# Kernel optimization log

Measured on AMD Instinct MI355X. Metric: run time of the kernel, lower is better.

The kernel has to match this reference:

```python
import jax, jax.numpy as jnp
import numpy as np
import math

B, T, Dm, H = 512, 64, 1024, 16
dh = Dm // H
CD, SD = 32, 256  # smolgen compress_dim, shared_dim
SCALE = 1.0 / math.sqrt(dh)
RES_SCALE = 1.0 / math.sqrt(2.0)  # n_layers=1
EPS = 1e-5


def _ln(v, g, b):
    m = jnp.mean(v, axis=-1, keepdims=True)
    var = jnp.mean(jnp.square(v - m), axis=-1, keepdims=True)
    return (v - m) * jax.lax.rsqrt(var + EPS) * g + b


def setup_inputs() -> dict:
    key = jax.random.key(0)
    ks = jax.random.split(key, 16)
    s = 0.02
    return {
        "x": jax.random.normal(ks[0], (B, T, Dm), jnp.float32),
        # weights stored (in, out); y = x @ W + b
        "Wq": jax.random.normal(ks[1], (Dm, Dm), jnp.float32) * s,
        "Wk": jax.random.normal(ks[2], (Dm, Dm), jnp.float32) * s,
        "Wv": jax.random.normal(ks[3], (Dm, Dm), jnp.float32) * s,
        "Wo_w": jax.random.normal(ks[4], (Dm, Dm), jnp.float32) * s,
        "Wo_b": jnp.zeros((Dm,), jnp.float32),
        "static_bias": jax.random.normal(ks[5], (H, T, T), jnp.float32) * s,
        "aQ": jax.random.normal(ks[6], (H, T, T, dh), jnp.float32) * s,
        "aK": jax.random.normal(ks[7], (H, T, T, dh), jnp.float32) * s,
        "aV": jax.random.normal(ks[8], (H, T, T, dh), jnp.float32) * s,
        # Smolgen params
        "pt_w": jax.random.normal(ks[9], (Dm, CD), jnp.float32) * s,
        "pt_b": jnp.zeros((CD,), jnp.float32),
        "pg_w": jax.random.normal(ks[10], (T * CD, SD), jnp.float32) * s,
        "pg_b": jnp.zeros((SD,), jnp.float32),
        "ph_w": jax.random.normal(ks[11], (SD, H * SD), jnp.float32) * s,
        "ph_b": jnp.zeros((H * SD,), jnp.float32),
        "ln1_g": jnp.ones((SD,), jnp.float32),
        "ln1_b": jnp.zeros((SD,), jnp.float32),
        "ln2_g": jnp.ones((SD,), jnp.float32),
        "ln2_b": jnp.zeros((SD,), jnp.float32),
        "shared_w": jax.random.normal(ks[12], (SD, T * T), jnp.float32) * s,
    }


def _smolgen(x, pt_w, pt_b, pg_w, pg_b, ph_w, ph_b, ln1_g, ln1_b, ln2_g, ln2_b, shared_w):
    z = x @ pt_w + pt_b                      # (B,T,CD)
    g = z.reshape(x.shape[0], T * CD) @ pg_w + pg_b  # (B,SD)
    g = _ln(jax.nn.silu(g), ln1_g, ln1_b)
    u = g @ ph_w + ph_b                      # (B,H*SD)
    u = jax.nn.silu(u).reshape(-1, H, SD)
    u = _ln(u, ln2_g, ln2_b)
    return (u @ shared_w).reshape(-1, H, T, T)


def reference(x, Wq, Wk, Wv, Wo_w, Wo_b, static_bias, aQ, aK, aV,
              pt_w, pt_b, pg_w, pg_b, ph_w, ph_b,
              ln1_g, ln1_b, ln2_g, ln2_b, shared_w):
    Bx = x.shape[0]
    Q = (x @ Wq).reshape(Bx, T, H, dh).transpose(0, 2, 1, 3)  # (B,H,T,dh)
    K = (x @ Wk).reshape(Bx, T, H, dh).transpose(0, 2, 1, 3)
    V = (x @ Wv).reshape(Bx, T, H, dh).transpose(0, 2, 1, 3)
    logits = jnp.einsum('bhtd,bhsd->bhts', Q, K) * SCALE
    logits = logits + static_bias[None]
    logits = logits + jnp.einsum('bhtd,htsd->bhts', Q, aK) * SCALE
    logits = logits + jnp.einsum('htsd,bhsd->bhts', aQ, K) * SCALE
    logits = logits + (jnp.einsum('htsd,htsd->hts', aQ, aK) * SCALE)[None]
    logits = logits + _smolgen(x, pt_w, pt_b, pg_w, pg_b, ph_w, ph_b,
                               ln1_g, ln1_b, ln2_g, ln2_b, shared_w)
    attn = jax.nn.softmax(logits, axis=-1)  # dropout = identity (eval mode)
    out = jnp.einsum('bhts,bhsd->bhtd', attn, V)
    out = out + jnp.einsum('bhts,htsd->bhtd', attn, aV)
    out = out.transpose(0, 2, 1, 3).reshape(Bx, T, Dm)
    return (out @ Wo_w + Wo_b) * RES_SCALE
```

## Files before the change

### kernel.cpp

```cpp
#include <hip/hip_runtime.h>
#include <cstdint>
#include <cstdio>

typedef unsigned short u16;
typedef __attribute__((ext_vector_type(8))) short s8v;
typedef __attribute__((ext_vector_type(4))) float f4v;
typedef __attribute__((ext_vector_type(4))) unsigned short u16x4;
typedef const __attribute__((address_space(1))) void* gas_p;
typedef __attribute__((address_space(3))) void* las_p;

#define DEV __device__ __forceinline__

static constexpr float SCALE_ = 0.125f;
static constexpr float RES_SCALE_ = 0.7071067811865475f;
static constexpr float EPS_ = 1e-5f;

DEV u16 f2bf(float f) {
  uint32_t u = __float_as_uint(f);
  u += 0x7fffu + ((u >> 16) & 1u);
  return (u16)(u >> 16);
}
DEV float bf2f(u16 h) { return __uint_as_float(((uint32_t)h) << 16); }

DEV f4v mfma16(s8v a, s8v b, f4v c) {
  return __builtin_amdgcn_mfma_f32_16x16x32_bf16(a, b, c, 0, 0, 0);
}

#define WAITVM4 asm volatile("s_waitcnt vmcnt(4)" ::: "memory")
#define WAITVM0 asm volatile("s_waitcnt vmcnt(0)" ::: "memory")
#define WAITLG0 asm volatile("s_waitcnt lgkmcnt(0)" ::: "memory")
#define SCHEDB  __builtin_amdgcn_sched_barrier(0)
#define BAR     __builtin_amdgcn_s_barrier()


__global__ void k_zero(float* __restrict__ p, long n) {
  long i = (long)blockIdx.x * blockDim.x + threadIdx.x;
  long stride = (long)gridDim.x * blockDim.x;
  for (; i < n; i += stride) p[i] = 0.f;
}

__global__ void k_cvt(const float* __restrict__ in, u16* __restrict__ out, long n4) {
  long i = (long)blockIdx.x * blockDim.x + threadIdx.x;
  long stride = (long)gridDim.x * blockDim.x;
  for (; i < n4; i += stride) {
    f4v v = *(const f4v*)&in[i * 4];
    u16x4 o;
    o.x = f2bf(v.x); o.y = f2bf(v.y); o.z = f2bf(v.z); o.w = f2bf(v.w);
    *(u16x4*)&out[i * 4] = o;
  }
}

__global__ void k_transpose(const float* __restrict__ in, u16* __restrict__ out, int K, int N) {
  __shared__ float tile[64][65];
  int kb = blockIdx.x * 64, nb = blockIdx.y * 64;
  for (int i = threadIdx.x; i < 4096; i += 256) {
    int r = i >> 6, c = i & 63;
    tile[r][c] = in[(long)(kb + r) * N + nb + c];
  }
  __syncthreads();
  for (int i = threadIdx.x; i < 4096; i += 256) {
    int c = i >> 6, r = i & 63;
    out[(long)(nb + c) * K + kb + r] = f2bf(tile[r][c]);
  }
}

__global__ void k_ptwt(const float* __restrict__ in, u16* __restrict__ out) {
  int idx = blockIdx.x * 256 + threadIdx.x;
  int n = idx >> 10, k = idx & 1023;
  out[idx] = f2bf(in[k * 32 + n]);
}

__global__ void k_avt(const float* __restrict__ aV, u16* __restrict__ aVt) {
  __shared__ float tile[64][65];
  int ht = blockIdx.x;
  const float* src = aV + (long)ht * 4096;
  for (int i = threadIdx.x; i < 4096; i += 256) {
    int s = i >> 6, d = i & 63;
    tile[s][d] = src[i];
  }
  __syncthreads();
  u16* dst = aVt + (long)ht * 4096;
  for (int i = threadIdx.x; i < 4096; i += 256) {
    int d = i >> 6, s = i & 63;
    dst[i] = f2bf(tile[s][d]);
  }
}

__global__ void k_extra(const float* __restrict__ sb, const float* __restrict__ aQ,
                        const float* __restrict__ aK, float* __restrict__ extra) {
  int idx = blockIdx.x * 256 + threadIdx.x;
  const float* q = aQ + (long)idx * 64;
  const float* k = aK + (long)idx * 64;
  float acc = 0.f;
#pragma unroll 8
  for (int d = 0; d < 64; d++) acc += q[d] * k[d];
  extra[idx] = sb[idx] + acc * SCALE_;
}

template <int EPI>
__launch_bounds__(512)
__global__ void k_gemm256(const u16* __restrict__ A, const u16* __restrict__ Bt,
                          void* __restrict__ Cv, const float* __restrict__ aux,
                          int M, int N, int K) {
  __shared__ u16 lds[65536];

  const int nwg = gridDim.x;
  int wg = blockIdx.x;
  if ((nwg & 7) == 0) wg = (wg & 7) * (nwg >> 3) + (wg >> 3);
  const int ntiles = N >> 8;
  const int mt = wg / ntiles, ntb = wg % ntiles;

  const int tid = threadIdx.x;
  const int lane = tid & 63, w = tid >> 6;
  const int wrB = (w >> 2) * 128, wcB = (w & 3) * 64;
  const int lr = lane & 15, lg = lane >> 4;
  const int hA = w >> 2;
  const int hB = (w & 3) >> 1;
  const int rB0 = (w & 1) * 64;
  const int xs0 = ((lg) ^ (lr & 7)) << 3;
  const int xs1 = ((4 + lg) ^ (lr & 7)) << 3;
  const int nt = K >> 6;

  const int sr = tid >> 3;
  const int sslot = (tid & 7) ^ (sr & 7);

#define GLOADA(tile, h)                                                          \
  do {                                                                           \
    const int bu_ = (tile) & 1;                                                  \
    const u16* s0_ = A + (long)(mt * 256 + (h) * 128 + sr) * K + (tile) * 64 + sslot * 8; \
    __builtin_amdgcn_global_load_lds((gas_p)s0_, (las_p)&lds[(bu_ * 2 + (h)) * 8192 + w * 512], 16, 0, 0); \
    const u16* s1_ = A + (long)(mt * 256 + (h) * 128 + 64 + sr) * K + (tile) * 64 + sslot * 8; \
    __builtin_amdgcn_global_load_lds((gas_p)s1_, (las_p)&lds[(bu_ * 2 + (h)) * 8192 + 4096 + w * 512], 16, 0, 0); \
  } while (0)

#define GLOADB(tile, h)                                                          \
  do {                                                                           \
    const int bu_ = (tile) & 1;                                                  \
    const u16* s0_ = Bt + (long)(ntb * 256 + (h) * 128 + sr) * K + (tile) * 64 + sslot * 8; \
    __builtin_amdgcn_global_load_lds((gas_p)s0_, (las_p)&lds[32768 + (bu_ * 2 + (h)) * 8192 + w * 512], 16, 0, 0); \
    const u16* s1_ = Bt + (long)(ntb * 256 + (h) * 128 + 64 + sr) * K + (tile) * 64 + sslot * 8; \
    __builtin_amdgcn_global_load_lds((gas_p)s1_, (las_p)&lds[32768 + (bu_ * 2 + (h)) * 8192 + 4096 + w * 512], 16, 0, 0); \
  } while (0)

  f4v acc[8][4];
#pragma unroll
  for (int mi = 0; mi < 8; mi++)
#pragma unroll
    for (int ni = 0; ni < 4; ni++) acc[mi][ni] = (f4v){0.f, 0.f, 0.f, 0.f};

  GLOADA(0, 0); GLOADA(0, 1);
  GLOADB(0, 0); GLOADB(0, 1);
  {
    const int t1 = (nt > 1) ? 1 : 0;
    GLOADB(t1, 0); GLOADB(t1, 1);
  }
  WAITVM0;
  BAR;

  s8v afr[4][2], bfr[4][2];

  for (int t = 0; t < nt; ++t) {
    const int bR = t & 1;
    const int aN = (t + 1 < nt) ? t + 1 : nt - 1;
    const int bN = (t + 2 < nt) ? t + 2 : nt - 1;
    const int aBase = (bR * 2 + hA) * 8192;
    const int bBase = 32768 + (bR * 2 + hB) * 8192;

#pragma unroll
    for (int mi = 0; mi < 4; mi++) {
      const int ro = (mi * 16 + lr) * 64;
      afr[mi][0] = *(const s8v*)&lds[aBase + ro + xs0];
      afr[mi][1] = *(const s8v*)&lds[aBase + ro + xs1];
    }
#pragma unroll
    for (int ni = 0; ni < 2; ni++) {
      const int ro = (rB0 + ni * 16 + lr) * 64;
      bfr[ni][0] = *(const s8v*)&lds[bBase + ro + xs0];
      bfr[ni][1] = *(const s8v*)&lds[bBase + ro + xs1];
    }
    GLOADA(aN, 0);
    SCHEDB; BAR; WAITLG0; SCHEDB;
    __builtin_amdgcn_s_setprio(1);
#pragma unroll
    for (int ks = 0; ks < 2; ks++)
#pragma unroll
      for (int mi = 0; mi < 4; mi++)
#pragma unroll
        for (int ni = 0; ni < 2; ni++)
          acc[mi][ni] = mfma16(afr[mi][ks], bfr[ni][ks], acc[mi][ni]);
    __builtin_amdgcn_s_setprio(0);
    BAR;

#pragma unroll
    for (int ni = 0; ni < 2; ni++) {
      const int ro = (rB0 + (2 + ni) * 16 + lr) * 64;
      bfr[2 + ni][0] = *(const s8v*)&lds[bBase + ro + xs0];
      bfr[2 + ni][1] = *(const s8v*)&lds[bBase + ro + xs1];
    }
    GLOADA(aN, 1);
    SCHEDB; BAR; WAITLG0; SCHEDB;
    __builtin_amdgcn_s_setprio(1);
#pragma unroll
    for (int ks = 0; ks < 2; ks++)
#pragma unroll
      for (int mi = 0; mi < 4; mi++)
#pragma unroll
        for (int ni = 2; ni < 4; ni++)
          acc[mi][ni] = mfma16(afr[mi][ks], bfr[ni][ks], acc[mi][ni]);
    __builtin_amdgcn_s_setprio(0);
    BAR;

#pragma unroll
    for (int mi = 0; mi < 4; mi++) {
      const int ro = ((64 + mi * 16) + lr) * 64;
      afr[mi][0] = *(const s8v*)&lds[aBase + ro + xs0];
      afr[mi][1] = *(const s8v*)&lds[aBase + ro + xs1];
    }
    GLOADB(bN, 0);
    SCHEDB; BAR; WAITLG0; SCHEDB;
    __builtin_amdgcn_s_setprio(1);
#pragma unroll
    for (int ks = 0; ks < 2; ks++)
#pragma unroll
      for (int mi = 0; mi < 4; mi++)
#pragma unroll
        for (int ni = 0; ni < 2; ni++)
          acc[4 + mi][ni] = mfma16(afr[mi][ks], bfr[ni][ks], acc[4 + mi][ni]);
    __builtin_amdgcn_s_setprio(0);
    BAR;

    GLOADB(bN, 1);
    SCHEDB; BAR;
    __builtin_amdgcn_s_setprio(1);
#pragma unroll
    for (int ks = 0; ks < 2; ks++)
#pragma unroll
      for (int mi = 0; mi < 4; mi++)
#pragma unroll
        for (int ni = 2; ni < 4; ni++)
          acc[4 + mi][ni] = mfma16(afr[mi][ks], bfr[ni][ks], acc[4 + mi][ni]);
    __builtin_amdgcn_s_setprio(0);
    WAITVM4; SCHEDB;
    BAR;
  }
#undef GLOADA
#undef GLOADB

  const int rbase = mt * 256 + wrB + lg * 4;
  const int cbase = ntb * 256 + wcB + lr;
  if (EPI == 0) {
    u16* C = (u16*)Cv;
#pragma unroll
    for (int mi = 0; mi < 8; mi++)
#pragma unroll
      for (int ni = 0; ni < 4; ni++)
#pragma unroll
        for (int j = 0; j < 4; j++)
          C[(long)(rbase + mi * 16 + j) * N + (cbase + ni * 16)] = f2bf(acc[mi][ni][j]);
  } else {
    float* C = (float*)Cv;
#pragma unroll
    for (int mi = 0; mi < 8; mi++)
#pragma unroll
      for (int ni = 0; ni < 4; ni++)
#pragma unroll
        for (int j = 0; j < 4; j++) {
          const int col = cbase + ni * 16;
          C[(long)(rbase + mi * 16 + j) * N + col] =
              (acc[mi][ni][j] + aux[col]) * RES_SCALE_;
        }
  }
}

template <int EPI>
__launch_bounds__(256)
__global__ void k_gemm(const u16* __restrict__ A, const u16* __restrict__ Bt,
                       void* __restrict__ Cv, const float* __restrict__ aux,
                       int M, int N, int K) {
  __shared__ u16 As[4096];
  __shared__ u16 Bs[4096];
  const int ntiles = N >> 7;
  const int mt = blockIdx.x / ntiles;
  const int nt = blockIdx.x % ntiles;
  const int tid = threadIdx.x;
  const int lane = tid & 63;
  const int w = tid >> 6;
  const int wr = w >> 1, wc = w & 1;
  const int lr = lane & 15, lg = lane >> 4;

  f4v acc[4][4];
#pragma unroll
  for (int m = 0; m < 4; m++)
#pragma unroll
    for (int n = 0; n < 4; n++) acc[m][n] = (f4v){0.f, 0.f, 0.f, 0.f};

  const u16* aSrc = A + (long)(mt * 128 + (tid >> 2)) * K + ((tid & 3) << 3);
  const u16* bSrc = Bt + (long)(nt * 128 + (tid >> 2)) * K + ((tid & 3) << 3);
  const long rowStep = (long)64 * K;

  const int kIters = K >> 5;
  for (int kb = 0; kb < kIters; kb++) {
    if (kb) __syncthreads();
    const u16* aP = aSrc + (kb << 5);
    const u16* bP = bSrc + (kb << 5);
    __builtin_amdgcn_global_load_lds((gas_p)aP, (las_p)&As[w * 512], 16, 0, 0);
    __builtin_amdgcn_global_load_lds((gas_p)(aP + rowStep), (las_p)&As[2048 + w * 512], 16, 0, 0);
    __builtin_amdgcn_global_load_lds((gas_p)bP, (las_p)&Bs[w * 512], 16, 0, 0);
    __builtin_amdgcn_global_load_lds((gas_p)(bP + rowStep), (las_p)&Bs[2048 + w * 512], 16, 0, 0);
    WAITVM0;
    __syncthreads();

    s8v af[4];
#pragma unroll
    for (int m = 0; m < 4; m++)
      af[m] = *(const s8v*)&As[(wr * 64 + m * 16 + lr) * 32 + (lg << 3)];
#pragma unroll
    for (int n = 0; n < 4; n++) {
      s8v bf = *(const s8v*)&Bs[(wc * 64 + n * 16 + lr) * 32 + (lg << 3)];
#pragma unroll
      for (int m = 0; m < 4; m++) acc[m][n] = mfma16(af[m], bf, acc[m][n]);
    }
  }

  const int rbase = mt * 128 + wr * 64 + lg * 4;
  const int cbase = nt * 128 + wc * 64 + lr;
  if (EPI == 1) {
    float* C = (float*)Cv;
#pragma unroll
    for (int m = 0; m < 4; m++)
#pragma unroll
      for (int n = 0; n < 4; n++)
#pragma unroll
        for (int j = 0; j < 4; j++) {
          int row = rbase + m * 16 + j;
          int col = cbase + n * 16;
          C[(long)row * N + col] = acc[m][n][j] + aux[col];
        }
  } else {
    u16* C = (u16*)Cv;
#pragma unroll
    for (int m = 0; m < 4; m++)
#pragma unroll
      for (int n = 0; n < 4; n++)
#pragma unroll
        for (int j = 0; j < 4; j++) {
          int row = rbase + m * 16 + j;
          int col = cbase + n * 16;
          C[(long)row * N + col] = f2bf(acc[m][n][j] + aux[((row & 15) << 12) | col]);
        }
  }
}


__launch_bounds__(256)
__global__ void k_smola_gemm(const u16* __restrict__ xbf, const u16* __restrict__ ptwT,
                             const float* __restrict__ ptb, u16* __restrict__ z) {
  const int rt = blockIdx.x;
  const int w = threadIdx.x >> 6, lane = threadIdx.x & 63;
  const int lr = lane & 15, lg = lane >> 4;
  const int row0 = rt * 64 + w * 16;
  f4v acc[2];
  acc[0] = (f4v){0.f, 0.f, 0.f, 0.f};
  acc[1] = (f4v){0.f, 0.f, 0.f, 0.f};
  const u16* aBase = xbf + (long)(row0 + lr) * 1024;
  const u16* bBase = ptwT + (long)lr * 1024;
#pragma unroll 4
  for (int k0 = 0; k0 < 1024; k0 += 32) {
    s8v a = *(const s8v*)&aBase[k0 + (lg << 3)];
#pragma unroll
    for (int n = 0; n < 2; n++) {
      s8v b = *(const s8v*)&bBase[(long)(n << 4) * 1024 + k0 + (lg << 3)];
      acc[n] = mfma16(a, b, acc[n]);
    }
  }
#pragma unroll
  for (int n = 0; n < 2; n++)
#pragma unroll
    for (int j = 0; j < 4; j++) {
      int col = (n << 4) + lr;
      z[(long)(row0 + lg * 4 + j) * 32 + col] = f2bf(acc[n][j] + ptb[col]);
    }
}

__launch_bounds__(64)
__global__ void k_smolb_gemm(const u16* __restrict__ z, const u16* __restrict__ pgwT,
                             const float* __restrict__ pgb, float* __restrict__ out) {
  const int bid = blockIdx.x;
  const int rt = bid >> 2, ct = bid & 3;
  const int lane = threadIdx.x;
  const int lr = lane & 15, lg = lane >> 4;
  f4v acc[4];
#pragma unroll
  for (int n = 0; n < 4; n++) acc[n] = (f4v){0.f, 0.f, 0.f, 0.f};
  const u16* aBase = z + (long)(rt * 16 + lr) * 2048;
  const u16* bBase = pgwT + (long)(ct * 64 + lr) * 2048;
#pragma unroll 4
  for (int k0 = 0; k0 < 2048; k0 += 32) {
    s8v a = *(const s8v*)&aBase[k0 + (lg << 3)];
#pragma unroll
    for (int n = 0; n < 4; n++) {
      s8v b = *(const s8v*)&bBase[(long)(n << 4) * 2048 + k0 + (lg << 3)];
      acc[n] = mfma16(a, b, acc[n]);
    }
  }
#pragma unroll
  for (int n = 0; n < 4; n++)
#pragma unroll
    for (int j = 0; j < 4; j++) {
      int row = rt * 16 + lg * 4 + j;
      int col = ct * 64 + (n << 4) + lr;
      out[(long)row * 256 + col] = acc[n][j] + pgb[col];
    }
}

__launch_bounds__(64)
__global__ void k_ln2(const float* __restrict__ uraw, const float* __restrict__ g2,
                      const float* __restrict__ b2, u16* __restrict__ ubf) {
  const int row = blockIdx.x;
  const int lane = threadIdx.x;
  f4v x = *(const f4v*)&uraw[(long)row * 256 + lane * 4];
  float v[4];
  float s = 0.f, q = 0.f;
#pragma unroll
  for (int j = 0; j < 4; j++) {
    float xx = x[j];
    v[j] = xx / (1.f + __expf(-xx));
    s += v[j]; q += v[j] * v[j];
  }
#pragma unroll
  for (int mk = 1; mk < 64; mk <<= 1) { s += __shfl_xor(s, mk); q += __shfl_xor(q, mk); }
  float mean = s * (1.f / 256.f);
  float var = q * (1.f / 256.f) - mean * mean;
  float rs = rsqrtf(var + EPS_);
  u16x4 o;
  float o0 = (v[0] - mean) * rs * g2[lane * 4 + 0] + b2[lane * 4 + 0];
  float o1 = (v[1] - mean) * rs * g2[lane * 4 + 1] + b2[lane * 4 + 1];
  float o2 = (v[2] - mean) * rs * g2[lane * 4 + 2] + b2[lane * 4 + 2];
  float o3 = (v[3] - mean) * rs * g2[lane * 4 + 3] + b2[lane * 4 + 3];
  o.x = f2bf(o0); o.y = f2bf(o1); o.z = f2bf(o2); o.w = f2bf(o3);
  *(u16x4*)&ubf[(long)row * 256 + lane * 4] = o;
}


__launch_bounds__(64)
__global__ void k_l2(const u16* __restrict__ qkv, const u16* __restrict__ aKb,
                     u16* __restrict__ l2b) {
  const int bid = blockIdx.x;
  const int bt = bid & 7, t = (bid >> 3) & 63, h = bid >> 9;
  const int lane = threadIdx.x;
  const int lr = lane & 15, lg = lane >> 4;
  f4v acc[4][4];
#pragma unroll
  for (int m = 0; m < 4; m++)
#pragma unroll
    for (int n = 0; n < 4; n++) acc[m][n] = (f4v){0.f, 0.f, 0.f, 0.f};
  const u16* qb = qkv + (long)t * 3072 + h * 64;
  const u16* kb = aKb + ((long)h * 64 + t) * 4096;
#pragma unroll
  for (int ks = 0; ks < 2; ks++) {
    s8v a[4], bb[4];
#pragma unroll
    for (int m = 0; m < 4; m++) {
      int brow = bt * 64 + m * 16 + lr;
      a[m] = *(const s8v*)&qb[(long)brow * 196608 + ks * 32 + (lg << 3)];
    }
#pragma unroll
    for (int n = 0; n < 4; n++)
      bb[n] = *(const s8v*)&kb[(n * 16 + lr) * 64 + ks * 32 + (lg << 3)];
#pragma unroll
    for (int m = 0; m < 4; m++)
#pragma unroll
      for (int n = 0; n < 4; n++) acc[m][n] = mfma16(a[m], bb[n], acc[m][n]);
  }
  u16* dst = l2b + ((long)h * 64 + t) * 32768;
#pragma unroll
  for (int m = 0; m < 4; m++)
#pragma unroll
    for (int n = 0; n < 4; n++)
#pragma unroll
      for (int j = 0; j < 4; j++) {
        int brow = bt * 64 + m * 16 + lg * 4 + j;
        int s = n * 16 + lr;
        dst[(long)brow * 64 + s] = f2bf(SCALE_ * acc[m][n][j]);
      }
}

__launch_bounds__(64)
__global__ void k_l3(const u16* __restrict__ qkv, const u16* __restrict__ aQb,
                     u16* __restrict__ l3a) {
  const int bid = blockIdx.x;
  const int bt = bid & 7, s = (bid >> 3) & 63, h = bid >> 9;
  const int lane = threadIdx.x;
  const int lr = lane & 15, lg = lane >> 4;
  f4v acc[4][4];
#pragma unroll
  for (int m = 0; m < 4; m++)
#pragma unroll
    for (int n = 0; n < 4; n++) acc[m][n] = (f4v){0.f, 0.f, 0.f, 0.f};
  const u16* kb = qkv + (long)s * 3072 + 1024 + h * 64;
  const u16* qb = aQb + (long)h * 262144 + (long)s * 64;
#pragma unroll
  for (int ks = 0; ks < 2; ks++) {
    s8v a[4], bb[4];
#pragma unroll
    for (int m = 0; m < 4; m++) {
      int brow = bt * 64 + m * 16 + lr;
      a[m] = *(const s8v*)&kb[(long)brow * 196608 + ks * 32 + (lg << 3)];
    }
#pragma unroll
    for (int n = 0; n < 4; n++) {
      int tc = n * 16 + lr;
      bb[n] = *(const s8v*)&qb[(long)tc * 4096 + ks * 32 + (lg << 3)];
    }
#pragma unroll
    for (int m = 0; m < 4; m++)
#pragma unroll
      for (int n = 0; n < 4; n++) acc[m][n] = mfma16(a[m], bb[n], acc[m][n]);
  }
#pragma unroll
  for (int m = 0; m < 4; m++)
#pragma unroll
    for (int n = 0; n < 4; n++)
#pragma unroll
      for (int j = 0; j < 4; j++) {
        int brow = bt * 64 + m * 16 + lg * 4 + j;
        int tc = n * 16 + lr;
        long idx = (((long)brow * 16 + h) * 64 + s) * 64 + tc;
        l3a[idx] = f2bf(SCALE_ * acc[m][n][j]);
      }
}

__launch_bounds__(64)
__global__ void k_c(const u16* __restrict__ attnb, const u16* __restrict__ aVt,
                    u16* __restrict__ outh) {
  const int bid = blockIdx.x;
  const int bt = bid & 7, t = (bid >> 3) & 63, h = bid >> 9;
  const int lane = threadIdx.x;
  const int lr = lane & 15, lg = lane >> 4;
  f4v acc[4][4];
#pragma unroll
  for (int m = 0; m < 4; m++)
#pragma unroll
    for (int n = 0; n < 4; n++) acc[m][n] = (f4v){0.f, 0.f, 0.f, 0.f};
  const u16* ab = attnb + ((long)h * 64 + t) * 64;
  const u16* vb = aVt + ((long)h * 64 + t) * 4096;
#pragma unroll
  for (int ks = 0; ks < 2; ks++) {
    s8v a[4], bb[4];
#pragma unroll
    for (int m = 0; m < 4; m++) {
      int brow = bt * 64 + m * 16 + lr;
      a[m] = *(const s8v*)&ab[(long)brow * 65536 + ks * 32 + (lg << 3)];
    }
#pragma unroll
    for (int n = 0; n < 4; n++)
      bb[n] = *(const s8v*)&vb[(n * 16 + lr) * 64 + ks * 32 + (lg << 3)];
#pragma unroll
    for (int m = 0; m < 4; m++)
#pragma unroll
      for (int n = 0; n < 4; n++) acc[m][n] = mfma16(a[m], bb[n], acc[m][n]);
  }
#pragma unroll
  for (int m = 0; m < 4; m++)
#pragma unroll
    for (int n = 0; n < 4; n++)
#pragma unroll
      for (int j = 0; j < 4; j++) {
        int brow = bt * 64 + m * 16 + lg * 4 + j;
        int d = n * 16 + lr;
        long idx = ((long)brow * 64 + t) * 1024 + h * 64 + d;
        outh[idx] = f2bf(bf2f(outh[idx]) + acc[m][n][j]);
      }
}

__launch_bounds__(256)
__global__ void k_attn(const u16* __restrict__ qkv, const u16* __restrict__ logits,
                       const u16* __restrict__ l2b, u16* __restrict__ l3a,
                       u16* __restrict__ outh) {
  __shared__ u16 Qs[64 * 72];
  __shared__ u16 Ks[64 * 72];
  __shared__ u16 Vt[64 * 72];
  __shared__ u16 Ps[64 * 72];
  const int bh = blockIdx.x;
  const int b = bh >> 4, h = bh & 15;
  const int tid = threadIdx.x;
  const int lane = tid & 63, w = tid >> 6;
  const int lr = lane & 15, lg = lane >> 4;
  const u16* qbase = qkv + (long)b * 196608 + h * 64;

#pragma unroll
  for (int c = 0; c < 2; c++) {
    int flat = c * 2048 + tid * 8;
    int row = flat >> 6, k = flat & 63;
    const u16* src = &qbase[(long)row * 3072 + k];
    *(s8v*)&Qs[row * 72 + k] = *(const s8v*)(src);
    *(s8v*)&Ks[row * 72 + k] = *(const s8v*)(src + 1024);
    s8v v = *(const s8v*)(src + 2048);
#pragma unroll
    for (int j = 0; j < 8; j++) Vt[(k + j) * 72 + row] = (u16)v[j];
  }
  __syncthreads();

  f4v sacc[4];
#pragma unroll
  for (int n = 0; n < 4; n++) sacc[n] = (f4v){0.f, 0.f, 0.f, 0.f};
#pragma unroll
  for (int ks = 0; ks < 2; ks++) {
    s8v a = *(const s8v*)&Qs[(w * 16 + lr) * 72 + ks * 32 + (lg << 3)];
#pragma unroll
    for (int n = 0; n < 4; n++) {
      s8v bb = *(const s8v*)&Ks[(n * 16 + lr) * 72 + ks * 32 + (lg << 3)];
      sacc[n] = mfma16(a, bb, sacc[n]);
    }
  }

  const long base = (long)bh * 4096;
  const int r0 = w * 16 + lg * 4;
  float p[4][4];
#pragma unroll
  for (int n = 0; n < 4; n++) {
    int s = n * 16 + lr;
    u16x4 l3v = *(const u16x4*)&l3a[base + s * 64 + r0];
#pragma unroll
    for (int j = 0; j < 4; j++) {
      float l3f = bf2f(((const u16*)&l3v)[j]);
      float l2f = bf2f(l2b[(((long)h * 64 + r0 + j) * 512 + b) * 64 + s]);
      float lgf = bf2f(logits[base + (r0 + j) * 64 + s]);
      p[n][j] = sacc[n][j] * SCALE_ + lgf + l3f + l2f;
    }
  }
#pragma unroll
  for (int j = 0; j < 4; j++) {
    float m = fmaxf(fmaxf(p[0][j], p[1][j]), fmaxf(p[2][j], p[3][j]));
    m = fmaxf(m, __shfl_xor(m, 1));
    m = fmaxf(m, __shfl_xor(m, 2));
    m = fmaxf(m, __shfl_xor(m, 4));
    m = fmaxf(m, __shfl_xor(m, 8));
    float s0 = 0.f;
#pragma unroll
    for (int n = 0; n < 4; n++) { p[n][j] = __expf(p[n][j] - m); s0 += p[n][j]; }
    s0 += __shfl_xor(s0, 1);
    s0 += __shfl_xor(s0, 2);
    s0 += __shfl_xor(s0, 4);
    s0 += __shfl_xor(s0, 8);
    float inv = 1.f / s0;
#pragma unroll
    for (int n = 0; n < 4; n++) p[n][j] *= inv;
  }

  __syncthreads();

#pragma unroll
  for (int n = 0; n < 4; n++) {
    int s = n * 16 + lr;
#pragma unroll
    for (int j = 0; j < 4; j++) {
      u16 pb = f2bf(p[n][j]);
      l3a[base + (r0 + j) * 64 + s] = pb;
      Ps[(r0 + j) * 72 + s] = pb;
    }
  }
  __syncthreads();

  f4v oacc[4];
#pragma unroll
  for (int n = 0; n < 4; n++) oacc[n] = (f4v){0.f, 0.f, 0.f, 0.f};
#pragma unroll
  for (int ks = 0; ks < 2; ks++) {
    s8v a = *(const s8v*)&Ps[(w * 16 + lr) * 72 + ks * 32 + (lg << 3)];
#pragma unroll
    for (int n = 0; n < 4; n++) {
      s8v vb = *(const s8v*)&Vt[(n * 16 + lr) * 72 + ks * 32 + (lg << 3)];
      oacc[n] = mfma16(a, vb, oacc[n]);
    }
  }
  u16* obase = outh + (long)b * 65536 + h * 64;
#pragma unroll
  for (int n = 0; n < 4; n++)
#pragma unroll
    for (int j = 0; j < 4; j++)
      obase[(long)(r0 + j) * 1024 + n * 16 + lr] = f2bf(oacc[n][j]);
}


extern "C" void kernel_launch(void* const* d_in, const int* in_sizes, int n_in,
                              void* d_out, int out_size, void* d_ws, size_t ws_size,
                              hipStream_t stream) {
  (void)in_sizes; (void)n_in;
  const float* x    = (const float*)d_in[0];
  const float* Wq   = (const float*)d_in[1];
  const float* Wk   = (const float*)d_in[2];
  const float* Wv   = (const float*)d_in[3];
  const float* Wo_w = (const float*)d_in[4];
  const float* Wo_b = (const float*)d_in[5];
  const float* sb   = (const float*)d_in[6];
  const float* aQ   = (const float*)d_in[7];
  const float* aK   = (const float*)d_in[8];
  const float* aV   = (const float*)d_in[9];
  const float* pt_w = (const float*)d_in[10];
  const float* pt_b = (const float*)d_in[11];
  const float* pg_w = (const float*)d_in[12];
  const float* pg_b = (const float*)d_in[13];
  const float* ph_w = (const float*)d_in[14];
  const float* ph_b = (const float*)d_in[15];
  const float* ln1g = (const float*)d_in[16];
  const float* ln1b = (const float*)d_in[17];
  const float* ln2g = (const float*)d_in[18];
  const float* ln2b = (const float*)d_in[19];
  const float* shw  = (const float*)d_in[20];

  char* wsp = (char*)d_ws;
  size_t off = 0;
  auto alloc = [&](size_t bytes) {
    void* p = wsp + off;
    off += (bytes + 255) & ~(size_t)255;
    return p;
  };
  u16*   xbf    = (u16*)alloc(33554432ull * 2);
  u16*   qkv    = (u16*)alloc(100663296ull * 2);
  u16*   logits = (u16*)alloc(33554432ull * 2);
  u16*   l3a    = (u16*)alloc(33554432ull * 2);
  u16*   l2b    = (u16*)alloc(33554432ull * 2);
  u16*   Wqkvt  = (u16*)alloc(3145728ull * 2);
  u16*   Wot    = (u16*)alloc(1048576ull * 2);
  u16*   phwt   = (u16*)alloc(1048576ull * 2);
  u16*   swt    = (u16*)alloc(1048576ull * 2);
  u16*   aKb    = (u16*)alloc(4194304ull * 2);
  u16*   aQb    = (u16*)alloc(4194304ull * 2);
  u16*   aVt    = (u16*)alloc(4194304ull * 2);
  float* extra  = (float*)alloc(65536ull * 4);
  u16*   z      = (u16*)alloc(1048576ull * 2);
  u16*   g      = (u16*)alloc(131072ull * 2);
  float* uraw   = (float*)alloc(2097152ull * 4);
  u16*   ubf    = (u16*)alloc(2097152ull * 2);
  u16*   ptwT   = (u16*)alloc(32768ull * 2);
  u16*   pgwT   = (u16*)alloc(524288ull * 2);
  float* uraw2  = (float*)alloc(131072ull * 4);
  u16*   outh   = xbf;
  float* dout   = (float*)d_out;

  if (off > ws_size) {
    fprintf(stderr, "[kernel_launch] insufficient workspace: need %zu have %zu\n",
            off, ws_size);
    k_zero<<<2048, 256, 0, stream>>>(dout, (long)out_size);
    return;
  }

  k_cvt<<<2048, 256, 0, stream>>>(x, xbf, 8388608);
  k_transpose<<<dim3(16, 16), 256, 0, stream>>>(Wq, Wqkvt, 1024, 1024);
  k_transpose<<<dim3(16, 16), 256, 0, stream>>>(Wk, Wqkvt + 1048576, 1024, 1024);
  k_transpose<<<dim3(16, 16), 256, 0, stream>>>(Wv, Wqkvt + 2097152, 1024, 1024);
  k_transpose<<<dim3(16, 16), 256, 0, stream>>>(Wo_w, Wot, 1024, 1024);
  k_transpose<<<dim3(4, 64), 256, 0, stream>>>(ph_w, phwt, 256, 4096);
  k_transpose<<<dim3(4, 64), 256, 0, stream>>>(shw, swt, 256, 4096);
  k_transpose<<<dim3(32, 4), 256, 0, stream>>>(pg_w, pgwT, 2048, 256);
  k_ptwt<<<128, 256, 0, stream>>>(pt_w, ptwT);
  k_cvt<<<2048, 256, 0, stream>>>(aK, aKb, 1048576);
  k_cvt<<<2048, 256, 0, stream>>>(aQ, aQb, 1048576);
  k_avt<<<1024, 256, 0, stream>>>(aV, aVt);
  k_extra<<<256, 256, 0, stream>>>(sb, aQ, aK, extra);

  k_gemm256<0><<<1536, 512, 0, stream>>>(xbf, Wqkvt, qkv, nullptr, 32768, 3072, 1024);

  k_smola_gemm<<<512, 256, 0, stream>>>(xbf, ptwT, pt_b, z);
  k_smolb_gemm<<<128, 64, 0, stream>>>(z, pgwT, pg_b, uraw2);
  k_ln2<<<512, 64, 0, stream>>>(uraw2, ln1g, ln1b, g);
  k_gemm<1><<<128, 256, 0, stream>>>(g, phwt, uraw, ph_b, 512, 4096, 256);
  k_ln2<<<8192, 64, 0, stream>>>(uraw, ln2g, ln2b, ubf);
  k_gemm<2><<<2048, 256, 0, stream>>>(ubf, swt, logits, extra, 8192, 4096, 256);

  k_l2<<<8192, 64, 0, stream>>>(qkv, aKb, l2b);
  k_l3<<<8192, 64, 0, stream>>>(qkv, aQb, l3a);
  k_attn<<<8192, 256, 0, stream>>>(qkv, logits, l2b, l3a, outh);
  k_c<<<8192, 64, 0, stream>>>(l3a, aVt, outh);
  k_gemm256<3><<<512, 512, 0, stream>>>(outh, Wot, dout, Wo_b, 32768, 1024, 1024);
}
```

Measured before the change: 768.7 us.

## Software-pipeline LDS fragment reads into MFMA phases of the GEMM main loop

Restructures the 256x256 bf16 GEMM inner loop so LDS fragment loads for the next phase, and for the next k-tile, are issued interleaved with the current MFMA groups instead of being waited on with explicit lgkmcnt(0) before each phase. B fragments are split into two register sets and the A fragments for the next tile are prefetched from the other LDS buffer at the end of each iteration. Global source addresses are also hoisted into precomputed base pointers. This relies on compiler-inserted waits for correctness and raises register pressure, and the reordered barriers may change hazards across the double buffer.

```diff
diff --git a/kernel.cpp b/kernel.cpp
--- a/kernel.cpp
+++ b/kernel.cpp
@@ -28,7 +28,6 @@
 
 #define WAITVM4 asm volatile("s_waitcnt vmcnt(4)" ::: "memory")
 #define WAITVM0 asm volatile("s_waitcnt vmcnt(0)" ::: "memory")
-#define WAITLG0 asm volatile("s_waitcnt lgkmcnt(0)" ::: "memory")
 #define SCHEDB  __builtin_amdgcn_sched_barrier(0)
 #define BAR     __builtin_amdgcn_s_barrier()
 
@@ -124,22 +123,25 @@
   const int sr = tid >> 3;
   const int sslot = (tid & 7) ^ (sr & 7);
 
+  const u16* aSrc = A + (long)(mt * 256 + sr) * K + sslot * 8;
+  const u16* bSrc = Bt + (long)(ntb * 256 + sr) * K + sslot * 8;
+  const long h128 = (long)128 * K;
+  const long r64 = (long)64 * K;
+
 #define GLOADA(tile, h)                                                          \
   do {                                                                           \
     const int bu_ = (tile) & 1;                                                  \
-    const u16* s0_ = A + (long)(mt * 256 + (h) * 128 + sr) * K + (tile) * 64 + sslot * 8; \
-    __builtin_amdgcn_global_load_lds((gas_p)s0_, (las_p)&lds[(bu_ * 2 + (h)) * 8192 + w * 512], 16, 0, 0); \
-    const u16* s1_ = A + (long)(mt * 256 + (h) * 128 + 64 + sr) * K + (tile) * 64 + sslot * 8; \
-    __builtin_amdgcn_global_load_lds((gas_p)s1_, (las_p)&lds[(bu_ * 2 + (h)) * 8192 + 4096 + w * 512], 16, 0, 0); \
+    const long o_ = (long)(tile) * 64 + (h) * h128;                              \
+    __builtin_amdgcn_global_load_lds((gas_p)(aSrc + o_), (las_p)&lds[(bu_ * 2 + (h)) * 8192 + w * 512], 16, 0, 0); \
+    __builtin_amdgcn_global_load_lds((gas_p)(aSrc + o_ + r64), (las_p)&lds[(bu_ * 2 + (h)) * 8192 + 4096 + w * 512], 16, 0, 0); \
   } while (0)
 
 #define GLOADB(tile, h)                                                          \
   do {                                                                           \
     const int bu_ = (tile) & 1;                                                  \
-    const u16* s0_ = Bt + (long)(ntb * 256 + (h) * 128 + sr) * K + (tile) * 64 + sslot * 8; \
-    __builtin_amdgcn_global_load_lds((gas_p)s0_, (las_p)&lds[32768 + (bu_ * 2 + (h)) * 8192 + w * 512], 16, 0, 0); \
-    const u16* s1_ = Bt + (long)(ntb * 256 + (h) * 128 + 64 + sr) * K + (tile) * 64 + sslot * 8; \
-    __builtin_amdgcn_global_load_lds((gas_p)s1_, (las_p)&lds[32768 + (bu_ * 2 + (h)) * 8192 + 4096 + w * 512], 16, 0, 0); \
+    const long o_ = (long)(tile) * 64 + (h) * h128;                              \
+    __builtin_amdgcn_global_load_lds((gas_p)(bSrc + o_), (las_p)&lds[32768 + (bu_ * 2 + (h)) * 8192 + w * 512], 16, 0, 0); \
+    __builtin_amdgcn_global_load_lds((gas_p)(bSrc + o_ + r64), (las_p)&lds[32768 + (bu_ * 2 + (h)) * 8192 + 4096 + w * 512], 16, 0, 0); \
   } while (0)
 
   f4v acc[8][4];
@@ -157,90 +159,110 @@
   WAITVM0;
   BAR;
 
-  s8v afr[4][2], bfr[4][2];
+  s8v AF[4][2], b01[2][2], b23[2][2];
+
+  {
+    const int aB0 = hA * 8192;
+    const int bB0 = 32768 + hB * 8192;
+#pragma unroll
+    for (int mi = 0; mi < 4; mi++) {
+      const int ro = (mi * 16 + lr) * 64;
+      AF[mi][0] = *(const s8v*)&lds[aB0 + ro + xs0];
+      AF[mi][1] = *(const s8v*)&lds[aB0 + ro + xs1];
+    }
+#pragma unroll
+    for (int ni = 0; ni < 2; ni++) {
+      const int ro = (rB0 + ni * 16 + lr) * 64;
+      b01[ni][0] = *(const s8v*)&lds[bB0 + ro + xs0];
+      b01[ni][1] = *(const s8v*)&lds[bB0 + ro + xs1];
+    }
+  }
+  SCHEDB;
 
   for (int t = 0; t < nt; ++t) {
-    const int bR = t & 1;
+    const int p = t & 1, q = p ^ 1;
     const int aN = (t + 1 < nt) ? t + 1 : nt - 1;
     const int bN = (t + 2 < nt) ? t + 2 : nt - 1;
-    const int aBase = (bR * 2 + hA) * 8192;
-    const int bBase = 32768 + (bR * 2 + hB) * 8192;
-
+    const int aBase = (p * 2 + hA) * 8192;
+    const int bBase = 32768 + (p * 2 + hB) * 8192;
+    const int aBaseN = (q * 2 + hA) * 8192;
+    const int bBaseN = 32768 + (q * 2 + hB) * 8192;
+
+#pragma unroll
+    for (int ni = 0; ni < 2; ni++) {
+      const int ro = (rB0 + (2 + ni) * 16 + lr) * 64;
+      b23[ni][0] = *(const s8v*)&lds[bBase + ro + xs0];
+      b23[ni][1] = *(const s8v*)&lds[bBase + ro + xs1];
+    }
+    SCHEDB;
+    GLOADA(aN, 0);
+    BAR;
+    __builtin_amdgcn_s_setprio(1);
+#pragma unroll
+    for (int mi = 0; mi < 4; mi++)
+#pragma unroll
+      for (int ks = 0; ks < 2; ks++)
+#pragma unroll
+        for (int ni = 0; ni < 2; ni++)
+          acc[mi][ni] = mfma16(AF[mi][ks], b01[ni][ks], acc[mi][ni]);
+    __builtin_amdgcn_s_setprio(0);
+    BAR;
+
+    GLOADA(aN, 1);
+    BAR;
+    __builtin_amdgcn_s_setprio(1);
 #pragma unroll
     for (int mi = 0; mi < 4; mi++) {
-      const int ro = (mi * 16 + lr) * 64;
-      afr[mi][0] = *(const s8v*)&lds[aBase + ro + xs0];
-      afr[mi][1] = *(const s8v*)&lds[aBase + ro + xs1];
-    }
+#pragma unroll
+      for (int ks = 0; ks < 2; ks++)
+#pragma unroll
+        for (int ni = 0; ni < 2; ni++)
+          acc[mi][2 + ni] = mfma16(AF[mi][ks], b23[ni][ks], acc[mi][2 + ni]);
+      const int ro = (64 + mi * 16 + lr) * 64;
+      AF[mi][0] = *(const s8v*)&lds[aBase + ro + xs0];
+      AF[mi][1] = *(const s8v*)&lds[aBase + ro + xs1];
+      SCHEDB;
+    }
+    __builtin_amdgcn_s_setprio(0);
+    BAR;
+
+    GLOADB(bN, 0);
+    BAR;
+    __builtin_amdgcn_s_setprio(1);
+#pragma unroll
+    for (int mi = 0; mi < 4; mi++)
+#pragma unroll
+      for (int ks = 0; ks < 2; ks++)
+#pragma unroll
+        for (int ni = 0; ni < 2; ni++)
+          acc[4 + mi][ni] = mfma16(AF[mi][ks], b01[ni][ks], acc[4 + mi][ni]);
+    __builtin_amdgcn_s_setprio(0);
+    BAR;
+
+    GLOADB(bN, 1);
+    WAITVM4;
+    BAR;
 #pragma unroll
     for (int ni = 0; ni < 2; ni++) {
       const int ro = (rB0 + ni * 16 + lr) * 64;
-      bfr[ni][0] = *(const s8v*)&lds[bBase + ro + xs0];
-      bfr[ni][1] = *(const s8v*)&lds[bBase + ro + xs1];
-    }
-    GLOADA(aN, 0);
-    SCHEDB; BAR; WAITLG0; SCHEDB;
+      b01[ni][0] = *(const s8v*)&lds[bBaseN + ro + xs0];
+      b01[ni][1] = *(const s8v*)&lds[bBaseN + ro + xs1];
+    }
+    SCHEDB;
     __builtin_amdgcn_s_setprio(1);
 #pragma unroll
-    for (int ks = 0; ks < 2; ks++)
-#pragma unroll
-      for (int mi = 0; mi < 4; mi++)
+    for (int mi = 0; mi < 4; mi++) {
+#pragma unroll
+      for (int ks = 0; ks < 2; ks++)
 #pragma unroll
         for (int ni = 0; ni < 2; ni++)
-          acc[mi][ni] = mfma16(afr[mi][ks], bfr[ni][ks], acc[mi][ni]);
+          acc[4 + mi][2 + ni] = mfma16(AF[mi][ks], b23[ni][ks], acc[4 + mi][2 + ni]);
+      const int ro = (mi * 16 + lr) * 64;
+      AF[mi][0] = *(const s8v*)&lds[aBaseN + ro + xs0];
+      AF[mi][1] = *(const s8v*)&lds[aBaseN + ro + xs1];
+      SCHEDB;
+    }
     __builtin_amdgcn_s_setprio(0);
-    BAR;
-
-#pragma unroll
-    for (int ni = 0; ni < 2; ni++) {
-      const int ro = (rB0 + (2 + ni) * 16 + lr) * 64;
-      bfr[2 + ni][0] = *(const s8v*)&lds[bBase + ro + xs0];
-      bfr[2 + ni][1] = *(const s8v*)&lds[bBase + ro + xs1];
-    }
-    GLOADA(aN, 1);
-    SCHEDB; BAR; WAITLG0; SCHEDB;
-    __builtin_amdgcn_s_setprio(1);
-#pragma unroll
-    for (int ks = 0; ks < 2; ks++)
-#pragma unroll
-      for (int mi = 0; mi < 4; mi++)
-#pragma unroll
-        for (int ni = 2; ni < 4; ni++)
-          acc[mi][ni] = mfma16(afr[mi][ks], bfr[ni][ks], acc[mi][ni]);
-    __builtin_amdgcn_s_setprio(0);
-    BAR;
-
-#pragma unroll
-    for (int mi = 0; mi < 4; mi++) {
-      const int ro = ((64 + mi * 16) + lr) * 64;
-      afr[mi][0] = *(const s8v*)&lds[aBase + ro + xs0];
-      afr[mi][1] = *(const s8v*)&lds[aBase + ro + xs1];
-    }
-    GLOADB(bN, 0);
-    SCHEDB; BAR; WAITLG0; SCHEDB;
-    __builtin_amdgcn_s_setprio(1);
-#pragma unroll
-    for (int ks = 0; ks < 2; ks++)
-#pragma unroll
-      for (int mi = 0; mi < 4; mi++)
-#pragma unroll
-        for (int ni = 0; ni < 2; ni++)
-          acc[4 + mi][ni] = mfma16(afr[mi][ks], bfr[ni][ks], acc[4 + mi][ni]);
-    __builtin_amdgcn_s_setprio(0);
-    BAR;
-
-    GLOADB(bN, 1);
-    SCHEDB; BAR;
-    __builtin_amdgcn_s_setprio(1);
-#pragma unroll
-    for (int ks = 0; ks < 2; ks++)
-#pragma unroll
-      for (int mi = 0; mi < 4; mi++)
-#pragma unroll
-        for (int ni = 2; ni < 4; ni++)
-          acc[4 + mi][ni] = mfma16(afr[mi][ks], bfr[ni][ks], acc[4 + mi][ni]);
-    __builtin_amdgcn_s_setprio(0);
-    WAITVM4; SCHEDB;
     BAR;
   }
 #undef GLOADA
```

Result: no change. 767.3 us (-0.2%).
